# Kernel optimization log

Measured on AMD Instinct MI355X. Metric: run time of the kernel, lower is better.

## Reference

```python
import jax, jax.numpy as jnp
import numpy as np

EPS = 1e-6

def masked_softmax(x, m, axis):
    # Faithful to KrantikariQA tensor_utils.masked_softmax:
    #   x = x*m; e = exp(x - max(x)) * m; e / (sum(e) + 1e-6)
    x = x * m
    ex = jnp.exp(x - jnp.max(x, axis=axis, keepdims=True)) * m
    return ex / (jnp.sum(ex, axis=axis, keepdims=True) + EPS)

def setup_inputs() -> dict:
    key = jax.random.key(0)
    k = jax.random.split(key, 7)
    Lq, Lp, B, D = 256, 256, 64, 1024
    q = jax.random.normal(k[0], (Lq, B, D), jnp.float32)
    p = jax.random.normal(k[1], (Lp, B, D), jnp.float32)
    qm = jax.random.randint(k[2], (B, Lq), 0, 2).astype(jnp.int32)
    pm = jax.random.randint(k[3], (B, Lp), 0, 2).astype(jnp.int32)
    # nn.Linear weights (out, in), no bias
    WF = jax.random.normal(k[4], (D, D), jnp.float32) * 0.02
    WG = jax.random.normal(k[5], (D, 2 * D), jnp.float32) * 0.02
    WH = jax.random.normal(k[6], (1, 2 * D), jnp.float32) * 0.02
    return {"q": q, "p": p, "qm": qm, "pm": pm, "WF": WF, "WG": WG, "WH": WH}

def reference(q, p, qm, pm, WF, WG, WH):
    # Attend: att = F(x), batch-first [B, L, D]
    att_q = jnp.einsum('lbd,ed->ble', q, WF)          # [B,Lq,D]
    att_p = jnp.einsum('lbd,ed->ble', p, WF)          # [B,Lp,D]
    e = jnp.einsum('bqe,bpe->bqp', att_q, att_p)      # [B,Lq,Lp]
    m = qm.astype(q.dtype)[:, :, None] * pm.astype(q.dtype)[:, None, :]  # [B,Lq,Lp]
    softmax_j = masked_softmax(e, m, axis=2)                              # over Lp
    softmax_i = masked_softmax(e.transpose(0, 2, 1), m.transpose(0, 2, 1), axis=2)  # [B,Lp,Lq]
    beta = jnp.einsum('bqp,pbd->bqd', softmax_j, p)   # [B,Lq,D]
    alpha = jnp.einsum('bpq,qbd->bpd', softmax_i, q)  # [B,Lp,D]
    # Compare
    v1 = jnp.concatenate([q.transpose(1, 0, 2), beta], axis=-1) @ WG.T   # [B,Lq,D]
    v2 = jnp.concatenate([p.transpose(1, 0, 2), alpha], axis=-1) @ WG.T  # [B,Lp,D]
    # Aggregate
    sum_v1 = jnp.sum(v1, axis=1)  # [B,D]
    sum_v2 = jnp.sum(v2, axis=1)  # [B,D]
    return jnp.concatenate([sum_v1, sum_v2], axis=-1) @ WH.T  # [B,1]
```

## Files before the change

kernel.cpp:

```cpp
#include <hip/hip_runtime.h>

typedef _Float16 f16x8 __attribute__((ext_vector_type(8)));
using f32x4 = __attribute__((ext_vector_type(4))) float;

constexpr int B = 64, L = 256, D = 1024;
constexpr int BD = B * D;
constexpr float EPS = 1e-6f;

__device__ __forceinline__ void gload_lds16(const void* g, void* l) {
    __builtin_amdgcn_global_load_lds((const __attribute__((address_space(1))) void*)g,
                                     (__attribute__((address_space(3))) void*)l,
                                     16, 0, 0);
}

__global__ __launch_bounds__(256) void k_wfgp(const float* __restrict__ WF,
                                              const float* __restrict__ WG,
                                              const float* __restrict__ WH,
                                              short* __restrict__ WFt16,
                                              float* __restrict__ gp1,
                                              float* __restrict__ gp2) {
    __shared__ float tile[32][33];
    const int bid = blockIdx.x;
    if (bid < 1024) {
        const int rt = bid >> 5, ct = bid & 31;
        const int t = threadIdx.x;
        const int r = t >> 3, c4 = (t & 7) * 4;
        float4 v = *(const float4*)(WF + (long)(rt * 32 + r) * D + ct * 32 + c4);
        tile[r][c4] = v.x; tile[r][c4 + 1] = v.y; tile[r][c4 + 2] = v.z; tile[r][c4 + 3] = v.w;
        __syncthreads();
        union { _Float16 h[4]; short4 s; } u;
        u.h[0] = (_Float16)tile[c4 + 0][r];
        u.h[1] = (_Float16)tile[c4 + 1][r];
        u.h[2] = (_Float16)tile[c4 + 2][r];
        u.h[3] = (_Float16)tile[c4 + 3][r];
        *(short4*)(WFt16 + (long)(ct * 32 + r) * D + rt * 32 + c4) = u.s;
    } else {
        const int lb = bid - 1024;
        const int kx = lb & 7, ec = lb >> 3;
        const int k = kx * 256 + threadIdx.x;
        const int e0 = ec * 128;
        float a = 0.f, c = 0.f;
        for (int e = 0; e < 128; ++e) {
            float w = WG[(long)(e0 + e) * (2 * D) + k];
            a += w * WH[e0 + e];
            c += w * WH[D + e0 + e];
        }
        gp1[ec * 2048 + k] = a; gp2[ec * 2048 + k] = c;
    }
}

template <int WM, int WN, int MR, int A32, int B32>
__global__ __launch_bounds__(WM * WN * 64) void k_gemm(
    const char* __restrict__ A, long sA, long bA,
    const char* __restrict__ Bm, long sB, long bB,
    int K, int bx, int per_batch, int f16_out,
    short* __restrict__ Ch, float* __restrict__ Cf, int ldC, long batchC)
{
    constexpr int BM = WM * MR * 16, BN = WN * 64;
    constexpr int T = WM * WN * 64;
    constexpr int TILEB = (BM + BN) * 128;
    constexpr int ROUNDS = TILEB / (T * 16);
    constexpr int ROUNDS_A = (BM * 128) / (T * 16);
    constexpr int R0 = A32 ? 0 : ROUNDS_A;
    constexpr int R1 = A32 ? ROUNDS_A : (B32 ? ROUNDS : ROUNDS_A);
    constexpr int NRS = (R1 > R0) ? (R1 - R0) : 1;
    __shared__ __align__(16) char lds[2 * TILEB];

    const int t = threadIdx.x, lane = t & 63, w = t >> 6;
    const int wm = w / WN, wn = w % WN;

    const int lin = blockIdx.x;
    const int chunk = gridDim.x >> 3;
    const int swz = (lin & 7) * chunk + (lin >> 3);
    const int z = swz / per_batch;
    const int r0_ = swz % per_batch;
    const int mb = (r0_ / bx) * BM, nb = (r0_ % bx) * BN;

    const char* Ab = A + bA * z;
    const char* Bb = Bm + bB * z;

    const char* sp[ROUNDS];
    #pragma unroll
    for (int r = 0; r < ROUNDS; ++r) {
        int g = r * T + t;
        int row = g >> 3, sg = g & 7;
        int lg = sg ^ (row & 7);
        if (r < ROUNDS_A) sp[r] = Ab + (long)(mb + row) * sA + lg * (A32 ? 32 : 16);
        else              sp[r] = Bb + (long)(nb + row - BM) * sB + lg * (B32 ? 32 : 16);
    }

    int aoff[MR][2], boff[4][2];
    #pragma unroll
    for (int i = 0; i < MR; ++i) {
        int ra = wm * (MR * 16) + i * 16 + (lane & 15);
        #pragma unroll
        for (int kh = 0; kh < 2; ++kh) {
            int c = (lane >> 4) + 4 * kh;
            aoff[i][kh] = ra * 128 + (c ^ (ra & 7)) * 16;
        }
    }
    #pragma unroll
    for (int j = 0; j < 4; ++j) {
        int rb = wn * 64 + j * 16 + (lane & 15);
        #pragma unroll
        for (int kh = 0; kh < 2; ++kh) {
            int c = (lane >> 4) + 4 * kh;
            boff[j][kh] = BM * 128 + rb * 128 + (c ^ (rb & 7)) * 16;
        }
    }

    f32x4 acc[MR][4] = {};
    const int NT = K >> 6;

    {
        #pragma unroll
        for (int r = 0; r < ROUNDS; ++r) {
            const bool is32 = (r < ROUNDS_A) ? (A32 != 0) : (B32 != 0);
            if (is32) {
                float4 s0 = *(const float4*)(sp[r]);
                float4 s1 = *(const float4*)(sp[r] + 16);
                union { _Float16 h[8]; int4 v; } u;
                u.h[0]=(_Float16)s0.x; u.h[1]=(_Float16)s0.y; u.h[2]=(_Float16)s0.z; u.h[3]=(_Float16)s0.w;
                u.h[4]=(_Float16)s1.x; u.h[5]=(_Float16)s1.y; u.h[6]=(_Float16)s1.z; u.h[7]=(_Float16)s1.w;
                *((int4*)(lds + (r * T + t) * 16)) = u.v;
            } else {
                gload_lds16(sp[r], lds + (r * T + t) * 16);
            }
        }
        asm volatile("s_waitcnt lgkmcnt(0)" ::: "memory");
    }

    int cur = 0;
    for (int kt = 0; kt < NT; ++kt) {
        asm volatile("s_waitcnt vmcnt(0)" ::: "memory");
        __builtin_amdgcn_s_barrier();
        float4 stg[NRS][2];
        char* dstb = lds + (cur ^ 1) * TILEB;
        if (kt + 1 < NT) {
            #pragma unroll
            for (int r = 0; r < ROUNDS; ++r) {
                const bool is32 = (r < ROUNDS_A) ? (A32 != 0) : (B32 != 0);
                if (is32) {
                    long kb = (long)(kt + 1) * 256;
                    stg[r - R0][0] = *(const float4*)(sp[r] + kb);
                    stg[r - R0][1] = *(const float4*)(sp[r] + kb + 16);
                } else {
                    long kb = (long)(kt + 1) * 128;
                    gload_lds16(sp[r] + kb, dstb + (r * T + t) * 16);
                }
            }
        }
        const char* lb = lds + cur * TILEB;
        #pragma unroll
        for (int kh = 0; kh < 2; ++kh) {
            f16x8 fb[4], fa[MR];
            #pragma unroll
            for (int j = 0; j < 4; ++j) fb[j] = *(const f16x8*)(lb + boff[j][kh]);
            #pragma unroll
            for (int i = 0; i < MR; ++i) fa[i] = *(const f16x8*)(lb + aoff[i][kh]);
            #pragma unroll
            for (int i = 0; i < MR; ++i)
                #pragma unroll
                for (int j = 0; j < 4; ++j)
                    acc[i][j] = __builtin_amdgcn_mfma_f32_16x16x32_f16(fb[j], fa[i], acc[i][j], 0, 0, 0);
        }
        if ((A32 || B32) && (kt + 1 < NT)) {
            #pragma unroll
            for (int r = R0; r < R1; ++r) {
                union { _Float16 h[8]; int4 v; } u;
                float4 s0 = stg[r - R0][0], s1 = stg[r - R0][1];
                u.h[0]=(_Float16)s0.x; u.h[1]=(_Float16)s0.y;
                u.h[2]=(_Float16)s0.z; u.h[3]=(_Float16)s0.w;
                u.h[4]=(_Float16)s1.x; u.h[5]=(_Float16)s1.y;
                u.h[6]=(_Float16)s1.z; u.h[7]=(_Float16)s1.w;
                *((int4*)(dstb + (r * T + t) * 16)) = u.v;
            }
            asm volatile("s_waitcnt lgkmcnt(0)" ::: "memory");
        }
        cur ^= 1;
    }

    const long zC = batchC * z;
    #pragma unroll
    for (int i = 0; i < MR; ++i)
        #pragma unroll
        for (int j = 0; j < 4; ++j) {
            int row = mb + wm * (MR * 16) + i * 16 + (lane & 15);
            int col = nb + wn * 64 + j * 16 + (lane >> 4) * 4;
            long idx = zC + (long)row * ldC + col;
            if (f16_out) {
                union { _Float16 h[4]; short4 s; } u;
                #pragma unroll
                for (int rr = 0; rr < 4; ++rr) u.h[rr] = (_Float16)acc[i][j][rr];
                *(short4*)(Ch + idx) = u.s;
            } else {
                float4 v = make_float4(acc[i][j][0], acc[i][j][1], acc[i][j][2], acc[i][j][3]);
                *(float4*)(Cf + idx) = v;
            }
        }
}

__global__ __launch_bounds__(256) void k_fold_g(const float* __restrict__ Gp,
                                                short* __restrict__ G16) {
    const int i = blockIdx.x * 256 + threadIdx.x;
    constexpr int N4 = (1 << 20) / 4;
    const float4* g = (const float4*)Gp;
    float4 v0 = g[i], v1 = g[N4 + i], v2 = g[2 * N4 + i], v3 = g[3 * N4 + i];
    union { _Float16 h[4]; short4 s; } u;
    u.h[0] = (_Float16)(v0.x + v1.x + v2.x + v3.x);
    u.h[1] = (_Float16)(v0.y + v1.y + v2.y + v3.y);
    u.h[2] = (_Float16)(v0.z + v1.z + v2.z + v3.z);
    u.h[3] = (_Float16)(v0.w + v1.w + v2.w + v3.w);
    ((short4*)G16)[i] = u.s;
}

__global__ __launch_bounds__(256) void k_pass1(const float* __restrict__ E,
                                               const int* __restrict__ qm,
                                               const int* __restrict__ pm,
                                               float* __restrict__ impart,
                                               float* __restrict__ ispart,
                                               float* __restrict__ cjpart) {
    const int qc = blockIdx.x, b = blockIdx.y;
    const int p = threadIdx.x, lane = p & 63, w = p >> 6;
    const int q0 = qc * 32;
    __shared__ float wred[32][4];
    __shared__ float rowmx[32], rowsm[32], qmv_s[32];
    if (p < 32) qmv_s[p] = (float)qm[b * L + q0 + p];
    __syncthreads();
    const float pmv = (float)pm[b * L + p];
    const float* eb = E + b * (L * L) + q0 * L + p;

    float xv[32];
    float im = -1e30f;
    #pragma unroll
    for (int r = 0; r < 32; ++r) {
        float mm = pmv * qmv_s[r];
        float x = eb[r * L] * mm;
        xv[r] = x;
        im = fmaxf(im, x);
        float v = x;
        #pragma unroll
        for (int o = 32; o; o >>= 1) v = fmaxf(v, __shfl_xor(v, o));
        if (lane == 0) wred[r][w] = v;
    }
    __syncthreads();
    if (p < 32) rowmx[p] = fmaxf(fmaxf(wred[p][0], wred[p][1]), fmaxf(wred[p][2], wred[p][3]));
    __syncthreads();
    float is = 0.f;
    #pragma unroll
    for (int r = 0; r < 32; ++r) {
        float mm = pmv * qmv_s[r];
        is += mm * __expf(xv[r] - im);
        float v = mm * __expf(xv[r] - rowmx[r]);
        #pragma unroll
        for (int o = 32; o; o >>= 1) v += __shfl_xor(v, o);
        if (lane == 0) wred[r][w] = v;
    }
    __syncthreads();
    if (p < 32) rowsm[p] = wred[p][0] + wred[p][1] + wred[p][2] + wred[p][3];
    __syncthreads();
    float cj = 0.f;
    #pragma unroll
    for (int r = 0; r < 32; ++r) {
        float mm = pmv * qmv_s[r];
        cj += mm * __expf(xv[r] - rowmx[r]) / (rowsm[r] + EPS);
    }
    const int o = (b * 8 + qc) * 256 + p;
    impart[o] = im; ispart[o] = is; cjpart[o] = cj;
}

__global__ __launch_bounds__(256) void k_combine(const float* __restrict__ impart,
                                                 const float* __restrict__ ispart,
                                                 const float* __restrict__ cjpart,
                                                 float* __restrict__ rmi,
                                                 float* __restrict__ rsi,
                                                 float* __restrict__ colj) {
    const int b = blockIdx.x, p = threadIdx.x;
    const int base = b * 8 * 256 + p;
    float m = -1e30f, s = 0.f, c = 0.f;
    #pragma unroll
    for (int k = 0; k < 8; ++k) m = fmaxf(m, impart[base + k * 256]);
    #pragma unroll
    for (int k = 0; k < 8; ++k) {
        s += ispart[base + k * 256] * __expf(impart[base + k * 256] - m);
        c += cjpart[base + k * 256];
    }
    rmi[b * L + p] = m; rsi[b * L + p] = s; colj[b * L + p] = c;
}

__global__ __launch_bounds__(256) void k_colsum_i(const float* __restrict__ E,
                                                  const int* __restrict__ qm,
                                                  const int* __restrict__ pm,
                                                  const float* __restrict__ rmaxi,
                                                  const float* __restrict__ rsumi,
                                                  float* __restrict__ coli) {
    const int wid = threadIdx.x >> 6, lane = threadIdx.x & 63;
    const int row = blockIdx.x * 4 + wid;
    const int b = row >> 8;
    const float qmv = (float)qm[row];
    const float* er = E + row * L;
    float acc = 0.f;
    #pragma unroll
    for (int i = 0; i < 4; ++i) {
        int pp = lane + 64 * i;
        float mm = qmv * (float)pm[b * L + pp];
        float x = er[pp] * mm;
        acc += mm * __expf(x - rmaxi[b * L + pp]) / (rsumi[b * L + pp] + EPS);
    }
    #pragma unroll
    for (int o = 32; o; o >>= 1) acc += __shfl_xor(acc, o);
    if (lane == 0) coli[row] = acc;
}

__global__ __launch_bounds__(128) void k_sums2(const float* __restrict__ Q,
                                               const float* __restrict__ P,
                                               const float* __restrict__ colj,
                                               const float* __restrict__ coli,
                                               float* __restrict__ pq,
                                               float* __restrict__ pp,
                                               float* __restrict__ pb,
                                               float* __restrict__ pa) {
    const int c = blockIdx.x, b = blockIdx.y, t = threadIdx.x;
    const int d0 = t * 8;
    float aq[8] = {}, ap[8] = {}, ab[8] = {}, aa[8] = {};
    for (int l = c * 16; l < c * 16 + 16; ++l) {
        const float* qp = Q + (long)l * BD + b * D + d0;
        const float* pp_ = P + (long)l * BD + b * D + d0;
        float4 q0 = *(const float4*)qp, q1 = *(const float4*)(qp + 4);
        float4 p0 = *(const float4*)pp_, p1 = *(const float4*)(pp_ + 4);
        float cj = colj[b * L + l], ci = coli[b * L + l];
        float qv[8] = {q0.x, q0.y, q0.z, q0.w, q1.x, q1.y, q1.z, q1.w};
        float pv[8] = {p0.x, p0.y, p0.z, p0.w, p1.x, p1.y, p1.z, p1.w};
        #pragma unroll
        for (int k = 0; k < 8; ++k) {
            aq[k] += qv[k]; ap[k] += pv[k]; ab[k] += cj * pv[k]; aa[k] += ci * qv[k];
        }
    }
    const long o = ((long)c * B + b) * D + d0;
    *(float4*)(pq + o) = make_float4(aq[0], aq[1], aq[2], aq[3]);
    *(float4*)(pq + o + 4) = make_float4(aq[4], aq[5], aq[6], aq[7]);
    *(float4*)(pp + o) = make_float4(ap[0], ap[1], ap[2], ap[3]);
    *(float4*)(pp + o + 4) = make_float4(ap[4], ap[5], ap[6], ap[7]);
    *(float4*)(pb + o) = make_float4(ab[0], ab[1], ab[2], ab[3]);
    *(float4*)(pb + o + 4) = make_float4(ab[4], ab[5], ab[6], ab[7]);
    *(float4*)(pa + o) = make_float4(aa[0], aa[1], aa[2], aa[3]);
    *(float4*)(pa + o + 4) = make_float4(aa[4], aa[5], aa[6], aa[7]);
}

__global__ __launch_bounds__(256) void k_final2(const float* __restrict__ pq,
                                                const float* __restrict__ pp,
                                                const float* __restrict__ pb,
                                                const float* __restrict__ pa,
                                                const float* __restrict__ gp1,
                                                const float* __restrict__ gp2,
                                                float* __restrict__ out) {
    const int b = blockIdx.x, t = threadIdx.x;
    float acc = 0.f;
    for (int d = t; d < D; d += 256) {
        float sq = 0.f, sp_ = 0.f, sb = 0.f, sa = 0.f;
        #pragma unroll
        for (int c2 = 0; c2 < 16; ++c2) {
            long o = ((long)c2 * B + b) * D + d;
            sq += pq[o]; sp_ += pp[o]; sb += pb[o]; sa += pa[o];
        }
        float g1d = 0.f, g1D = 0.f, g2d = 0.f, g2D = 0.f;
        #pragma unroll
        for (int ec = 0; ec < 8; ++ec) {
            g1d += gp1[ec * 2048 + d];     g1D += gp1[ec * 2048 + D + d];
            g2d += gp2[ec * 2048 + d];     g2D += gp2[ec * 2048 + D + d];
        }
        acc += sq * g1d + sb * g1D + sp_ * g2d + sa * g2D;
    }
    #pragma unroll
    for (int o = 32; o; o >>= 1) acc += __shfl_xor(acc, o);
    __shared__ float red[4];
    const int wid = t >> 6, lane = t & 63;
    if (lane == 0) red[wid] = acc;
    __syncthreads();
    if (t == 0) out[b] = red[0] + red[1] + red[2] + red[3];
}

extern "C" void kernel_launch(void* const* d_in, const int* in_sizes, int n_in,
                              void* d_out, int out_size, void* d_ws, size_t ws_size,
                              hipStream_t stream) {
    const float* q  = (const float*)d_in[0];
    const float* p  = (const float*)d_in[1];
    const int*   qm = (const int*)d_in[2];
    const int*   pm = (const int*)d_in[3];
    const float* WF = (const float*)d_in[4];
    const float* WG = (const float*)d_in[5];
    const float* WH = (const float*)d_in[6];
    float* out = (float*)d_out;

    char* wsb = (char*)d_ws;
    short* T16   = (short*)(wsb);
    short* WFt16 = (short*)(wsb + (32l << 20));
    short* G16   = (short*)(wsb + (34l << 20));
    float* Gp    = (float*)(wsb + (36l << 20));
    float* E     = (float*)(wsb + (36l << 20));
    float* st    = (float*)(wsb + (52l << 20));
    const int BL = B * L;
    float* impart = st;                  float* ispart = impart + B * 8 * 256;
    float* cjpart = ispart + B * 8 * 256;
    float* rmi  = cjpart + B * 8 * 256;  float* rsi  = rmi + BL;
    float* colj = rsi + BL;              float* coli = colj + BL;
    float* pq   = coli + BL;             float* pp   = pq + 16 * BD;
    float* pb   = pp + 16 * BD;          float* pa   = pb + 16 * BD;
    float* gp1  = pa + 16 * BD;          float* gp2  = gp1 + 8 * 2048;

    k_wfgp<<<1088, 256, 0, stream>>>(WF, WG, WH, WFt16, gp1, gp2);
    k_gemm<2, 2, 4, 0, 0><<<256, 256, 0, stream>>>(
        (const char*)WFt16, 2048, 512, (const char*)WFt16, 2048, 512,
        256, 8, 64, 0, nullptr, Gp, 1024, 1l << 20);
    k_fold_g<<<1024, 256, 0, stream>>>(Gp, G16);
    k_gemm<2, 4, 8, 1, 0><<<256, 512, 0, stream>>>(
        (const char*)q, 4096, 0, (const char*)G16, 2048, 0,
        1024, 4, 256, 1, T16, nullptr, 1024, 0);
    k_gemm<2, 2, 4, 0, 1><<<256, 256, 0, stream>>>(
        (const char*)T16, 64l * 2048, 2048, (const char*)p, 64l * 4096, 4096,
        1024, 2, 4, 0, nullptr, E, 256, 65536);
    k_pass1<<<dim3(8, B), 256, 0, stream>>>(E, qm, pm, impart, ispart, cjpart);
    k_combine<<<B, 256, 0, stream>>>(impart, ispart, cjpart, rmi, rsi, colj);
    k_colsum_i<<<BL / 4, 256, 0, stream>>>(E, qm, pm, rmi, rsi, coli);
    k_sums2<<<dim3(16, B), 128, 0, stream>>>(q, p, colj, coli, pq, pp, pb, pa);
    k_final2<<<B, 256, 0, stream>>>(pq, pp, pb, pa, gp1, gp2, out);
}
```

Measured before the change: 160.2 us.

## Add dedicated triple-buffered q·G GEMM kernel with register-staged fp32 conversion

Replaces the generic templated GEMM for the q×G product with a specialized kernel using 256x128 tiles, a three-stage LDS ring, and a block-index swizzle. The fp32 A operand is loaded into registers two tiles ahead and converted to fp16 before being written to LDS. The B tile is streamed with direct global-to-LDS loads. The aim is to overlap global loads with MFMA work and to improve cache locality, at the cost of a large LDS footprint that limits occupancy to one block per CU.

```diff
diff --git a/kernel.cpp b/kernel.cpp
--- a/kernel.cpp
+++ b/kernel.cpp
@@ -49,6 +49,156 @@
     }
 }
 
+__global__ __launch_bounds__(512, 1) void k_qG8(const char* __restrict__ Aq,
+                                                const char* __restrict__ Bg,
+                                                short* __restrict__ Ch) {
+    constexpr int TILEB = 49152;
+    __shared__ __align__(16) char lds[3 * TILEB];
+    const int t = threadIdx.x, lane = t & 63, w = t >> 6;
+    const int wm = w >> 1, wn = w & 1;
+
+    const int lin = blockIdx.x;
+    const int swz = (lin & 7) * 64 + (lin >> 3);
+    const int mb = (swz >> 3) * 256, nb = (swz & 7) * 128;
+
+    const char* spA[4];
+    #pragma unroll
+    for (int r = 0; r < 4; ++r) {
+        int g = r * 512 + t;
+        int row = g >> 3, sg = g & 7;
+        spA[r] = Aq + (long)(mb + row) * 4096 + (sg ^ (row & 7)) * 32;
+    }
+    const char* spB[2];
+    #pragma unroll
+    for (int r = 0; r < 2; ++r) {
+        int g = r * 512 + t;
+        int row = g >> 3, sg = g & 7;
+        spB[r] = Bg + (long)(nb + row) * 2048 + (sg ^ (row & 7)) * 16;
+    }
+
+    int aoff[4][2], boff[4][2];
+    #pragma unroll
+    for (int i = 0; i < 4; ++i) {
+        int ra = wm * 64 + i * 16 + (lane & 15);
+        #pragma unroll
+        for (int kh = 0; kh < 2; ++kh) {
+            int c = (lane >> 4) + 4 * kh;
+            aoff[i][kh] = ra * 128 + ((c ^ (ra & 7))) * 16;
+        }
+    }
+    #pragma unroll
+    for (int j = 0; j < 4; ++j) {
+        int rb = wn * 64 + j * 16 + (lane & 15);
+        #pragma unroll
+        for (int kh = 0; kh < 2; ++kh) {
+            int c = (lane >> 4) + 4 * kh;
+            boff[j][kh] = 32768 + rb * 128 + ((c ^ (rb & 7))) * 16;
+        }
+    }
+
+    f32x4 acc[4][4] = {};
+    constexpr int NT = 16;
+    float4 rsE[4][2], rsO[4][2];
+
+#define QG_LOADA(KT, RS)                                                    \
+    {                                                                       \
+        long kb = (long)(KT) * 256;                                         \
+        _Pragma("unroll")                                                   \
+        for (int r = 0; r < 4; ++r) {                                       \
+            RS[r][0] = *(const float4*)(spA[r] + kb);                       \
+            RS[r][1] = *(const float4*)(spA[r] + kb + 16);                  \
+        }                                                                   \
+    }
+#define QG_LOADB(KT)                                                        \
+    {                                                                       \
+        long kb = (long)(KT) * 128;                                         \
+        char* dstb = lds + ((KT) % 3) * TILEB + 32768;                      \
+        _Pragma("unroll")                                                   \
+        for (int r = 0; r < 2; ++r)                                         \
+            gload_lds16(spB[r] + kb, dstb + (r * 512 + t) * 16);            \
+    }
+#define QG_WRITEA(KT, RS)                                                   \
+    {                                                                       \
+        char* dstb = lds + ((KT) % 3) * TILEB;                              \
+        _Pragma("unroll")                                                   \
+        for (int r = 0; r < 4; ++r) {                                       \
+            union { _Float16 h[8]; int4 v; } u;                             \
+            float4 s0 = RS[r][0], s1 = RS[r][1];                            \
+            u.h[0]=(_Float16)s0.x; u.h[1]=(_Float16)s0.y;                   \
+            u.h[2]=(_Float16)s0.z; u.h[3]=(_Float16)s0.w;                   \
+            u.h[4]=(_Float16)s1.x; u.h[5]=(_Float16)s1.y;                   \
+            u.h[6]=(_Float16)s1.z; u.h[7]=(_Float16)s1.w;                   \
+            *((int4*)(dstb + (r * 512 + t) * 16)) = u.v;                    \
+        }                                                                   \
+    }
+#define QG_MFMA(KT, KH)                                                     \
+    {                                                                       \
+        const char* lb = lds + ((KT) % 3) * TILEB;                          \
+        f16x8 fb[4], fa[4];                                                 \
+        _Pragma("unroll")                                                   \
+        for (int j = 0; j < 4; ++j) fb[j] = *(const f16x8*)(lb + boff[j][KH]); \
+        _Pragma("unroll")                                                   \
+        for (int i = 0; i < 4; ++i) fa[i] = *(const f16x8*)(lb + aoff[i][KH]); \
+        __builtin_amdgcn_s_setprio(1);                                      \
+        _Pragma("unroll")                                                   \
+        for (int i = 0; i < 4; ++i)                                         \
+            _Pragma("unroll")                                               \
+            for (int j = 0; j < 4; ++j)                                     \
+                acc[i][j] = __builtin_amdgcn_mfma_f32_16x16x32_f16(         \
+                    fb[j], fa[i], acc[i][j], 0, 0, 0);                      \
+        __builtin_amdgcn_s_setprio(0);                                      \
+    }
+#define QG_ITER(KT, RSLOAD, RSWRITE)                                        \
+    {                                                                       \
+                                                                   \
+        if ((KT) + 2 < NT) { QG_LOADB((KT) + 2) QG_LOADA((KT) + 2, RSLOAD) }\
+        QG_MFMA(KT, 0)                                                      \
+        __builtin_amdgcn_s_barrier();                                       \
+                                                                   \
+        QG_MFMA(KT, 1)                                                      \
+        if ((KT) + 1 < NT) {                                                \
+            QG_WRITEA((KT) + 1, RSWRITE)                                    \
+            asm volatile("s_waitcnt lgkmcnt(0)" ::: "memory");              \
+        }                                                                   \
+        if ((KT) + 2 < NT)                                                  \
+            asm volatile("s_waitcnt vmcnt(10)" ::: "memory");               \
+        else                                                                \
+            asm volatile("s_waitcnt vmcnt(0)" ::: "memory");                \
+        __builtin_amdgcn_s_barrier();                                       \
+    }
+
+    QG_LOADB(0)
+    QG_LOADA(0, rsE)
+    QG_WRITEA(0, rsE)
+    QG_LOADB(1)
+    QG_LOADA(1, rsO)
+    asm volatile("s_waitcnt lgkmcnt(0)" ::: "memory");
+    asm volatile("s_waitcnt vmcnt(10)" ::: "memory");
+    __builtin_amdgcn_s_barrier();
+
+    for (int kt = 0; kt < NT; kt += 2) {
+        QG_ITER(kt, rsE, rsO)
+        QG_ITER(kt + 1, rsO, rsE)
+    }
+#undef QG_ITER
+#undef QG_MFMA
+#undef QG_WRITEA
+#undef QG_LOADB
+#undef QG_LOADA
+
+    #pragma unroll
+    for (int i = 0; i < 4; ++i)
+        #pragma unroll
+        for (int j = 0; j < 4; ++j) {
+            int row = mb + wm * 64 + i * 16 + (lane & 15);
+            int col = nb + wn * 64 + j * 16 + (lane >> 4) * 4;
+            union { _Float16 h[4]; short4 s; } u;
+            #pragma unroll
+            for (int rr = 0; rr < 4; ++rr) u.h[rr] = (_Float16)acc[i][j][rr];
+            *(short4*)(Ch + (long)row * 1024 + col) = u.s;
+        }
+}
+
 template <int WM, int WN, int MR, int A32, int B32>
 __global__ __launch_bounds__(WM * WN * 64) void k_gemm(
     const char* __restrict__ A, long sA, long bA,
@@ -413,9 +563,7 @@
         (const char*)WFt16, 2048, 512, (const char*)WFt16, 2048, 512,
         256, 8, 64, 0, nullptr, Gp, 1024, 1l << 20);
     k_fold_g<<<1024, 256, 0, stream>>>(Gp, G16);
-    k_gemm<2, 4, 8, 1, 0><<<256, 512, 0, stream>>>(
-        (const char*)q, 4096, 0, (const char*)G16, 2048, 0,
-        1024, 4, 256, 1, T16, nullptr, 1024, 0);
+    k_qG8<<<512, 512, 0, stream>>>((const char*)q, (const char*)G16, T16);
     k_gemm<2, 2, 4, 0, 1><<<256, 256, 0, stream>>>(
         (const char*)T16, 64l * 2048, 2048, (const char*)p, 64l * 4096, 4096,
         1024, 2, 4, 0, nullptr, E, 256, 65536);
```

After: 172.5 us. 7.7% more time.
